# Kernel optimization log

Measured on AMD Instinct MI355X. Metric: run time of the kernel, lower is better.

The kernel has to match this reference:

```python
import jax, jax.numpy as jnp
import numpy as np
import math

N, L, S, H, E, D = 2, 2048, 2048, 16, 64, 64

def setup_inputs() -> dict:
    key = jax.random.key(0)
    kq, kk, kv = jax.random.split(key, 3)
    return {
        "queries": jax.random.normal(kq, (N, L, H, E), dtype=jnp.float32),
        "keys": jax.random.normal(kk, (N, S, H, E), dtype=jnp.float32),
        "values": jax.random.normal(kv, (N, S, H, D), dtype=jnp.float32),
        "attn_mask": jnp.zeros((L, S), dtype=jnp.float32),  # additive mask
    }

def reference(queries, keys, values, attn_mask):
    e = queries.shape[-1]
    softmax_temp = 1.0 / math.sqrt(e)  # self.softmax_temp is None -> 1/sqrt(E)
    # (N,L,H,E) x (N,S,H,E) -> (N,H,L,S)
    qk = jnp.einsum('nlhe,nshe->nhls', queries, keys)
    qk = qk + attn_mask  # additive mask broadcast over (N,H)
    att = jax.nn.softmax(softmax_temp * qk, axis=-1)
    # dropout rate 0.0 (eval) -> identity
    v = jnp.einsum('nhls,nshd->nlhd', att, values)
    return v
```

## Files before the change

### kernel.cpp

```cpp
#include <hip/hip_runtime.h>
#include <hip/hip_bf16.h>


typedef short bf16x8 __attribute__((ext_vector_type(8)));
typedef short short4v __attribute__((ext_vector_type(4)));
typedef unsigned uint2v __attribute__((ext_vector_type(2)));
typedef float f32x4 __attribute__((ext_vector_type(4)));

constexpr int Nb = 2, Lq = 2048, Sk = 2048, Hh = 16, Ee = 64, Dd = 64;
constexpr int BM = 128;
constexpr int BN = 64;
constexpr int NT = Sk / BN;
constexpr int KVB = Nb * Hh * NT * 16 * 64 / 256;
constexpr float SCALE_LOG2E = 0.125f * 1.4426950408889634f;

__device__ __forceinline__ short f2bf(float f) {
  union { float f; unsigned u; } v; v.f = f;
  unsigned r = (v.u + 0x7fffu + ((v.u >> 16) & 1u)) >> 16;
  return (short)r;
}

__device__ __forceinline__ unsigned pack_bf16x2(float a, float b) {
  union { __hip_bfloat162 h; unsigned u; } v;
  float2 f; f.x = a; f.y = b;
  v.h = __float22bfloat162_rn(f);
  return v.u;
}

__device__ __forceinline__ float bf_lo(unsigned u) { return __uint_as_float(u << 16); }
__device__ __forceinline__ float bf_hi(unsigned u) { return __uint_as_float(u & 0xffff0000u); }

__device__ __forceinline__ void async_copy16(const void* g, void* l) {
  __builtin_amdgcn_global_load_lds(
      (const __attribute__((address_space(1))) unsigned int*)g,
      (__attribute__((address_space(3))) unsigned int*)l, 16, 0, 0);
}

__global__ __launch_bounds__(256) void prep_all(const float* __restrict__ K,
                                                const float* __restrict__ V,
                                                const float* __restrict__ M,
                                                short* __restrict__ KVf,
                                                short* __restrict__ Mg) {
  if (blockIdx.x < KVB) {
    int gid = blockIdx.x * 256 + threadIdx.x;
    int l = gid & 63;
    int chunkid = gid >> 6;
    int ch = chunkid & 15;
    int t  = (chunkid >> 4) & 31;
    int nh = chunkid >> 9;
    int n = nh >> 4, h = nh & 15;
    int c = l & 15, quad = l >> 4;
    bf16x8 o;
    if (ch < 8) {
      int sb = ch >> 1, kc = ch & 1;
      int s = t * 64 + sb * 16 + c;
      int e0 = kc * 32 + quad * 8;
      const float* p = K + (((size_t)n * Sk + s) * Hh + h) * Ee + e0;
      float4 x = *(const float4*)(p);
      float4 y = *(const float4*)(p + 4);
      o[0] = f2bf(x.x); o[1] = f2bf(x.y); o[2] = f2bf(x.z); o[3] = f2bf(x.w);
      o[4] = f2bf(y.x); o[5] = f2bf(y.y); o[6] = f2bf(y.z); o[7] = f2bf(y.w);
    } else {
      int db = (ch - 8) >> 1, kc = (ch - 8) & 1;
      int d = db * 16 + c;
      int s0 = t * 64 + kc * 32 + quad * 8;
      const float* p = V + (((size_t)n * Sk + s0) * Hh + h) * Dd + d;
#pragma unroll
      for (int j = 0; j < 8; ++j) o[j] = f2bf(p[(size_t)j * Hh * Dd]);
    }
    *(bf16x8*)(KVf + (size_t)gid * 8) = o;
  } else {
    int u = (blockIdx.x - KVB) * 256 + threadIdx.x;
    int colg = u & 511;
    int row  = u >> 9;
    int qt = row >> 7, wv = (row >> 5) & 3, cb = (row >> 4) & 1, cc = row & 15;
    int t = colg >> 4, sb = (colg >> 2) & 3, quad = colg & 3;
    int lane = quad * 16 + cc;
    float4 mv = *(const float4*)(M + (size_t)row * Sk + colg * 4);
    short4v o;
    o[0] = f2bf(mv.x * SCALE_LOG2E); o[1] = f2bf(mv.y * SCALE_LOG2E);
    o[2] = f2bf(mv.z * SCALE_LOG2E); o[3] = f2bf(mv.w * SCALE_LOG2E);
    size_t gran = ((((size_t)((qt * 4 + wv) * 2 + cb) * 32 + t) * 4 + sb) * 64) + lane;
    *(short4v*)(Mg + gran * 4) = o;
  }
}

template <int NS>
__global__ __launch_bounds__(256, 4) void attn_fwd(
    const float* __restrict__ Q, const short* __restrict__ KVf,
    const short* __restrict__ Mg, float* __restrict__ P0,
    float* __restrict__ P1, float* __restrict__ rsW)
{
  __shared__ short KV[2][8192];
  __shared__ short Ps[4][1024];

  const int tid  = threadIdx.x;
  const int lane = tid & 63;
  const int w    = tid >> 6;
  const int quad = lane >> 4;
  const int c    = lane & 15;

  const int id   = blockIdx.x;
  const int slot = id >> 3;
  const int nh   = (id & 7) * 4 + (slot & 3);
  const int qt   = (slot >> 2) & 15;
  const int sp   = (NS == 2) ? (slot >> 6) : 0;
  const int n    = nh >> 4;
  const int h    = nh & 15;

  const int row0 = qt * BM + w * 32;
  const int t0 = sp * (NT / NS), tc = NT / NS;

  bf16x8 qfrag[2][2];
#pragma unroll
  for (int cb = 0; cb < 2; ++cb) {
    const float* qp = Q + (((size_t)n * Lq + (row0 + cb * 16 + c)) * Hh + h) * Ee;
#pragma unroll
    for (int kc = 0; kc < 2; ++kc) {
      const float* p = qp + kc * 32 + quad * 8;
      float4 x = *(const float4*)(p);
      float4 y = *(const float4*)(p + 4);
      bf16x8 f;
      f[0] = f2bf(x.x * SCALE_LOG2E); f[1] = f2bf(x.y * SCALE_LOG2E);
      f[2] = f2bf(x.z * SCALE_LOG2E); f[3] = f2bf(x.w * SCALE_LOG2E);
      f[4] = f2bf(y.x * SCALE_LOG2E); f[5] = f2bf(y.y * SCALE_LOG2E);
      f[6] = f2bf(y.z * SCALE_LOG2E); f[7] = f2bf(y.w * SCALE_LOG2E);
      qfrag[cb][kc] = f;
    }
  }

  f32x4 o[2][4];
#pragma unroll
  for (int cb = 0; cb < 2; ++cb)
#pragma unroll
    for (int db = 0; db < 4; ++db) { o[cb][db][0] = 0.f; o[cb][db][1] = 0.f; o[cb][db][2] = 0.f; o[cb][db][3] = 0.f; }
  float rs[2] = {0.f, 0.f};

  const short* kvt = KVf + (size_t)nh * NT * 8192;
  const short* mbase = Mg + (size_t)((qt * 4 + w) * 2) * 32768 + lane * 4;

#pragma unroll
  for (int i = 0; i < 4; ++i) {
    int ch = w * 4 + i;
    async_copy16(kvt + ((size_t)t0 * 8192) + ch * 512 + lane * 8, &KV[0][ch * 512 + lane * 8]);
  }
  __syncthreads();

  for (int tt = 0; tt < tc; ++tt) {
    const int t = t0 + tt;
    const int buf = tt & 1;

    uint2v mv[2][4];
#pragma unroll
    for (int cb = 0; cb < 2; ++cb)
#pragma unroll
      for (int sb = 0; sb < 4; ++sb)
        mv[cb][sb] = *(const uint2v*)(mbase + ((size_t)cb * 32 + t) * 1024 + sb * 256);

    if (tt + 1 < tc) {
      const short* gk = kvt + (size_t)(t + 1) * 8192;
#pragma unroll
      for (int i = 0; i < 4; ++i) {
        int ch = w * 4 + i;
        async_copy16(gk + ch * 512 + lane * 8, &KV[buf ^ 1][ch * 512 + lane * 8]);
      }
    }

    const short* kb = &KV[buf][0];

    f32x4 sacc[2][4];
#pragma unroll
    for (int cb = 0; cb < 2; ++cb)
#pragma unroll
      for (int sb = 0; sb < 4; ++sb) { sacc[cb][sb][0] = 0.f; sacc[cb][sb][1] = 0.f; sacc[cb][sb][2] = 0.f; sacc[cb][sb][3] = 0.f; }
#pragma unroll
    for (int kc = 0; kc < 2; ++kc) {
#pragma unroll
      for (int sb = 0; sb < 4; ++sb) {
        bf16x8 kfrag = *(const bf16x8*)&kb[(sb * 2 + kc) * 512 + lane * 8];
#pragma unroll
        for (int cb = 0; cb < 2; ++cb)
          sacc[cb][sb] = __builtin_amdgcn_mfma_f32_16x16x32_bf16(kfrag, qfrag[cb][kc], sacc[cb][sb], 0, 0, 0);
      }
    }

    bf16x8 pfrag[2][2];
#pragma unroll
    for (int cb = 0; cb < 2; ++cb) {
#pragma unroll
      for (int sb = 0; sb < 4; ++sb) {
        float p0 = __builtin_amdgcn_exp2f(sacc[cb][sb][0] + bf_lo(mv[cb][sb].x));
        float p1 = __builtin_amdgcn_exp2f(sacc[cb][sb][1] + bf_hi(mv[cb][sb].x));
        float p2 = __builtin_amdgcn_exp2f(sacc[cb][sb][2] + bf_lo(mv[cb][sb].y));
        float p3 = __builtin_amdgcn_exp2f(sacc[cb][sb][3] + bf_hi(mv[cb][sb].y));
        rs[cb] += (p0 + p1) + (p2 + p3);
        uint2v pv;
        pv.x = pack_bf16x2(p0, p1);
        pv.y = pack_bf16x2(p2, p3);
        int gp = ((4 * sb + quad) ^ c) * 4;
        *(uint2v*)&Ps[w][c * 64 + gp] = pv;
      }
#pragma unroll
      for (int kc = 0; kc < 2; ++kc) {
        int G0 = 8 * kc + 2 * quad;
        int ga = (G0 ^ c) * 4, gb = ((G0 + 1) ^ c) * 4;
        union { uint2v u[2]; bf16x8 f; } uu;
        uu.u[0] = *(const uint2v*)&Ps[w][c * 64 + ga];
        uu.u[1] = *(const uint2v*)&Ps[w][c * 64 + gb];
        pfrag[cb][kc] = uu.f;
      }
    }

#pragma unroll
    for (int kc = 0; kc < 2; ++kc) {
#pragma unroll
      for (int db = 0; db < 4; ++db) {
        bf16x8 vfrag = *(const bf16x8*)&kb[(8 + db * 2 + kc) * 512 + lane * 8];
#pragma unroll
        for (int cb = 0; cb < 2; ++cb)
          o[cb][db] = __builtin_amdgcn_mfma_f32_16x16x32_bf16(vfrag, pfrag[cb][kc], o[cb][db], 0, 0, 0);
      }
    }

    __syncthreads();
  }

  float* P = (sp == 0) ? P0 : P1;
#pragma unroll
  for (int cb = 0; cb < 2; ++cb) {
    float v = rs[cb];
    v += __shfl_xor(v, 16, 64);
    v += __shfl_xor(v, 32, 64);
    const int qrow = row0 + cb * 16 + c;
    if (quad == 0) rsW[(size_t)sp * 65536 + nh * 2048 + qrow] = v;
    float* op = P + (((size_t)n * Lq + qrow) * Hh + h) * Dd + quad * 4;
#pragma unroll
    for (int db = 0; db < 4; ++db) {
      float4 ov;
      ov.x = o[cb][db][0]; ov.y = o[cb][db][1];
      ov.z = o[cb][db][2]; ov.w = o[cb][db][3];
      *(float4*)(op + db * 16) = ov;
    }
  }
}

template <int NS>
__global__ __launch_bounds__(256) void combine(float* __restrict__ Out,
                                               const float* __restrict__ P1,
                                               const float* __restrict__ rsW) {
  int gid = blockIdx.x * 256 + threadIdx.x;
  size_t i4 = (size_t)gid * 4;
  int hh = (int)((i4 >> 6) & 15);
  int l  = (int)((i4 >> 10) & 2047);
  int nn = (int)(i4 >> 21);
  int nh = nn * 16 + hh;
  float rs = rsW[nh * 2048 + l];
  float4 v = *(const float4*)(Out + i4);
  if (NS == 2) {
    rs += rsW[65536 + (size_t)nh * 2048 + l];
    float4 b = *(const float4*)(P1 + i4);
    v.x += b.x; v.y += b.y; v.z += b.z; v.w += b.w;
  }
  float inv = 1.0f / rs;
  v.x *= inv; v.y *= inv; v.z *= inv; v.w *= inv;
  *(float4*)(Out + i4) = v;
}

extern "C" void kernel_launch(void* const* d_in, const int* in_sizes, int n_in,
                              void* d_out, int out_size, void* d_ws, size_t ws_size,
                              hipStream_t stream) {
  const float* Q   = (const float*)d_in[0];
  const float* K   = (const float*)d_in[1];
  const float* V   = (const float*)d_in[2];
  const float* Msk = (const float*)d_in[3];
  float* Out = (float*)d_out;

  short* KVf = (short*)d_ws;
  short* Mg  = KVf + (size_t)8388608;
  float* rsW = (float*)(Mg + (size_t)4194304);
  float* P1  = rsW + 131072;

  const size_t need2 = 16777216u + 8388608u + 524288u + 16777216u;
  const bool split = ws_size >= need2;

  prep_all<<<dim3(KVB + 4096), dim3(256), 0, stream>>>(K, V, Msk, KVf, Mg);

  if (split) {
    attn_fwd<2><<<dim3(1024), dim3(256), 0, stream>>>(Q, KVf, Mg, Out, P1, rsW);
    combine<2><<<dim3(4096), dim3(256), 0, stream>>>(Out, P1, rsW);
  } else {
    attn_fwd<1><<<dim3(512), dim3(256), 0, stream>>>(Q, KVf, Mg, Out, P1, rsW);
    combine<1><<<dim3(4096), dim3(256), 0, stream>>>(Out, P1, rsW);
  }
}
```

Before: 171.0 us.

## Drop LDS round-trip for P by using 16x16x16 MFMA and relayout V/mask

The PV product now uses the 16x16x16 bf16 MFMA, so the exponentiated score accumulator fragments feed directly as the B operand. This removes the per-wave LDS staging buffer for P and its write/read shuffle. The V and mask prep layouts are rearranged to match. The mask is now preloaded into the score accumulators as the initial value and prefetched one tile ahead into registers. The cost is twice as many smaller MFMA instructions for PV and more registers held by the mask prefetch.

Result: faster. 166.3 us (-2.8%).

```diff
diff --git a/kernel.cpp b/kernel.cpp
--- a/kernel.cpp
+++ b/kernel.cpp
@@ -5,13 +5,15 @@
 typedef short bf16x8 __attribute__((ext_vector_type(8)));
 typedef short short4v __attribute__((ext_vector_type(4)));
 typedef unsigned uint2v __attribute__((ext_vector_type(2)));
+typedef unsigned uint4v __attribute__((ext_vector_type(4)));
 typedef float f32x4 __attribute__((ext_vector_type(4)));
 
 constexpr int Nb = 2, Lq = 2048, Sk = 2048, Hh = 16, Ee = 64, Dd = 64;
 constexpr int BM = 128;
 constexpr int BN = 64;
 constexpr int NT = Sk / BN;
-constexpr int KVB = Nb * Hh * NT * 16 * 64 / 256;
+constexpr int KVB = 4096;
+constexpr int MSKB = 2048;
 constexpr float SCALE_LOG2E = 0.125f * 1.4426950408889634f;
 
 __device__ __forceinline__ short f2bf(float f) {
@@ -43,45 +45,59 @@
                                                 short* __restrict__ Mg) {
   if (blockIdx.x < KVB) {
     int gid = blockIdx.x * 256 + threadIdx.x;
-    int l = gid & 63;
-    int chunkid = gid >> 6;
-    int ch = chunkid & 15;
-    int t  = (chunkid >> 4) & 31;
-    int nh = chunkid >> 9;
+    int off8 = gid & 1023;
+    int t  = (gid >> 10) & 31;
+    int nh = gid >> 15;
     int n = nh >> 4, h = nh & 15;
-    int c = l & 15, quad = l >> 4;
-    bf16x8 o;
-    if (ch < 8) {
-      int sb = ch >> 1, kc = ch & 1;
-      int s = t * 64 + sb * 16 + c;
-      int e0 = kc * 32 + quad * 8;
-      const float* p = K + (((size_t)n * Sk + s) * Hh + h) * Ee + e0;
+    short* dst = KVf + ((size_t)(nh * NT + t)) * 8192 + off8 * 8;
+    if (off8 < 512) {
+      int ch = off8 >> 6;
+      int l  = off8 & 63;
+      int sb = ch >> 1, kc = ch & 1, c = l & 15, quad = l >> 4;
+      const float* p = K + (((size_t)n * Sk + (t * 64 + sb * 16 + c)) * Hh + h) * Ee
+                         + kc * 32 + quad * 8;
       float4 x = *(const float4*)(p);
       float4 y = *(const float4*)(p + 4);
+      bf16x8 o;
       o[0] = f2bf(x.x); o[1] = f2bf(x.y); o[2] = f2bf(x.z); o[3] = f2bf(x.w);
       o[4] = f2bf(y.x); o[5] = f2bf(y.y); o[6] = f2bf(y.z); o[7] = f2bf(y.w);
+      *(bf16x8*)dst = o;
     } else {
-      int db = (ch - 8) >> 1, kc = (ch - 8) & 1;
-      int d = db * 16 + c;
-      int s0 = t * 64 + kc * 32 + quad * 8;
-      const float* p = V + (((size_t)n * Sk + s0) * Hh + h) * Dd + d;
-#pragma unroll
-      for (int j = 0; j < 8; ++j) o[j] = f2bf(p[(size_t)j * Hh * Dd]);
-    }
-    *(bf16x8*)(KVf + (size_t)gid * 8) = o;
+      int pos = off8 - 512;
+      int vch = pos >> 5;
+      int l0  = (pos & 31) * 2;
+      int db = vch >> 2, sb = vch & 3;
+      bf16x8 o;
+#pragma unroll
+      for (int i = 0; i < 2; ++i) {
+        int l = l0 + i, c = l & 15, quad = l >> 4;
+        const float* p = V + (((size_t)n * Sk + (t * 64 + sb * 16 + quad * 4)) * Hh + h) * Dd
+                           + db * 16 + c;
+#pragma unroll
+        for (int j = 0; j < 4; ++j) o[i * 4 + j] = f2bf(p[(size_t)j * Hh * Dd]);
+      }
+      *(bf16x8*)dst = o;
+    }
   } else {
     int u = (blockIdx.x - KVB) * 256 + threadIdx.x;
-    int colg = u & 511;
-    int row  = u >> 9;
-    int qt = row >> 7, wv = (row >> 5) & 3, cb = (row >> 4) & 1, cc = row & 15;
-    int t = colg >> 4, sb = (colg >> 2) & 3, quad = colg & 3;
-    int lane = quad * 16 + cc;
-    float4 mv = *(const float4*)(M + (size_t)row * Sk + colg * 4);
-    short4v o;
-    o[0] = f2bf(mv.x * SCALE_LOG2E); o[1] = f2bf(mv.y * SCALE_LOG2E);
-    o[2] = f2bf(mv.z * SCALE_LOG2E); o[3] = f2bf(mv.w * SCALE_LOG2E);
-    size_t gran = ((((size_t)((qt * 4 + wv) * 2 + cb) * 32 + t) * 4 + sb) * 64) + lane;
-    *(short4v*)(Mg + gran * 4) = o;
+    int sub  = u & 3;
+    int lane = (u >> 2) & 63;
+    int t    = (u >> 8) & 31;
+    int qw   = u >> 13;
+    int cb = sub >> 1, sbp = sub & 1;
+    int c = lane & 15, quad = lane >> 4;
+    int row = (qw >> 2) * 128 + (qw & 3) * 32 + cb * 16 + c;
+    short o[8];
+#pragma unroll
+    for (int k = 0; k < 2; ++k) {
+      int sb = sbp * 2 + k;
+      float4 mv = *(const float4*)(M + (size_t)row * Sk + t * 64 + sb * 16 + quad * 4);
+      o[k * 4 + 0] = f2bf(mv.x * SCALE_LOG2E);
+      o[k * 4 + 1] = f2bf(mv.y * SCALE_LOG2E);
+      o[k * 4 + 2] = f2bf(mv.z * SCALE_LOG2E);
+      o[k * 4 + 3] = f2bf(mv.w * SCALE_LOG2E);
+    }
+    *(bf16x8*)(Mg + (size_t)u * 8) = *(const bf16x8*)o;
   }
 }
 
@@ -92,7 +108,6 @@
     float* __restrict__ P1, float* __restrict__ rsW)
 {
   __shared__ short KV[2][8192];
-  __shared__ short Ps[4][1024];
 
   const int tid  = threadIdx.x;
   const int lane = tid & 63;
@@ -137,42 +152,48 @@
   float rs[2] = {0.f, 0.f};
 
   const short* kvt = KVf + (size_t)nh * NT * 8192;
-  const short* mbase = Mg + (size_t)((qt * 4 + w) * 2) * 32768 + lane * 4;
+  const short* mbase = Mg + (size_t)(qt * 4 + w) * 65536 + lane * 32;
 
 #pragma unroll
   for (int i = 0; i < 4; ++i) {
-    int ch = w * 4 + i;
-    async_copy16(kvt + ((size_t)t0 * 8192) + ch * 512 + lane * 8, &KV[0][ch * 512 + lane * 8]);
-  }
+    int seg = w * 4 + i;
+    async_copy16(kvt + ((size_t)t0 * 8192) + seg * 512 + lane * 8, &KV[0][seg * 512 + lane * 8]);
+  }
+  uint4v mcur[4], mnxt[4];
+#pragma unroll
+  for (int i = 0; i < 4; ++i) mcur[i] = *(const uint4v*)(mbase + (size_t)t0 * 2048 + i * 8);
   __syncthreads();
 
   for (int tt = 0; tt < tc; ++tt) {
     const int t = t0 + tt;
     const int buf = tt & 1;
 
-    uint2v mv[2][4];
+    if (tt + 1 < tc) {
+      const short* gm = mbase + (size_t)(t + 1) * 2048;
+#pragma unroll
+      for (int i = 0; i < 4; ++i) mnxt[i] = *(const uint4v*)(gm + i * 8);
+      const short* gk = kvt + (size_t)(t + 1) * 8192;
+#pragma unroll
+      for (int i = 0; i < 4; ++i) {
+        int seg = w * 4 + i;
+        async_copy16(gk + seg * 512 + lane * 8, &KV[buf ^ 1][seg * 512 + lane * 8]);
+      }
+    }
+
+    const short* kb = &KV[buf][0];
+
+    f32x4 sacc[2][4];
 #pragma unroll
     for (int cb = 0; cb < 2; ++cb)
 #pragma unroll
-      for (int sb = 0; sb < 4; ++sb)
-        mv[cb][sb] = *(const uint2v*)(mbase + ((size_t)cb * 32 + t) * 1024 + sb * 256);
-
-    if (tt + 1 < tc) {
-      const short* gk = kvt + (size_t)(t + 1) * 8192;
-#pragma unroll
-      for (int i = 0; i < 4; ++i) {
-        int ch = w * 4 + i;
-        async_copy16(gk + ch * 512 + lane * 8, &KV[buf ^ 1][ch * 512 + lane * 8]);
-      }
-    }
-
-    const short* kb = &KV[buf][0];
-
-    f32x4 sacc[2][4];
-#pragma unroll
-    for (int cb = 0; cb < 2; ++cb)
-#pragma unroll
-      for (int sb = 0; sb < 4; ++sb) { sacc[cb][sb][0] = 0.f; sacc[cb][sb][1] = 0.f; sacc[cb][sb][2] = 0.f; sacc[cb][sb][3] = 0.f; }
+      for (int sbp = 0; sbp < 2; ++sbp) {
+        uint4v m = mcur[cb * 2 + sbp];
+        sacc[cb][sbp * 2 + 0][0] = bf_lo(m.x); sacc[cb][sbp * 2 + 0][1] = bf_hi(m.x);
+        sacc[cb][sbp * 2 + 0][2] = bf_lo(m.y); sacc[cb][sbp * 2 + 0][3] = bf_hi(m.y);
+        sacc[cb][sbp * 2 + 1][0] = bf_lo(m.z); sacc[cb][sbp * 2 + 1][1] = bf_hi(m.z);
+        sacc[cb][sbp * 2 + 1][2] = bf_lo(m.w); sacc[cb][sbp * 2 + 1][3] = bf_hi(m.w);
+      }
+
 #pragma unroll
     for (int kc = 0; kc < 2; ++kc) {
 #pragma unroll
@@ -184,45 +205,36 @@
       }
     }
 
-    bf16x8 pfrag[2][2];
-#pragma unroll
-    for (int cb = 0; cb < 2; ++cb) {
+    short4v pv[2][4];
+#pragma unroll
+    for (int cb = 0; cb < 2; ++cb)
 #pragma unroll
       for (int sb = 0; sb < 4; ++sb) {
-        float p0 = __builtin_amdgcn_exp2f(sacc[cb][sb][0] + bf_lo(mv[cb][sb].x));
-        float p1 = __builtin_amdgcn_exp2f(sacc[cb][sb][1] + bf_hi(mv[cb][sb].x));
-        float p2 = __builtin_amdgcn_exp2f(sacc[cb][sb][2] + bf_lo(mv[cb][sb].y));
-        float p3 = __builtin_amdgcn_exp2f(sacc[cb][sb][3] + bf_hi(mv[cb][sb].y));
+        float p0 = __builtin_amdgcn_exp2f(sacc[cb][sb][0]);
+        float p1 = __builtin_amdgcn_exp2f(sacc[cb][sb][1]);
+        float p2 = __builtin_amdgcn_exp2f(sacc[cb][sb][2]);
+        float p3 = __builtin_amdgcn_exp2f(sacc[cb][sb][3]);
         rs[cb] += (p0 + p1) + (p2 + p3);
-        uint2v pv;
-        pv.x = pack_bf16x2(p0, p1);
-        pv.y = pack_bf16x2(p2, p3);
-        int gp = ((4 * sb + quad) ^ c) * 4;
-        *(uint2v*)&Ps[w][c * 64 + gp] = pv;
-      }
-#pragma unroll
-      for (int kc = 0; kc < 2; ++kc) {
-        int G0 = 8 * kc + 2 * quad;
-        int ga = (G0 ^ c) * 4, gb = ((G0 + 1) ^ c) * 4;
-        union { uint2v u[2]; bf16x8 f; } uu;
-        uu.u[0] = *(const uint2v*)&Ps[w][c * 64 + ga];
-        uu.u[1] = *(const uint2v*)&Ps[w][c * 64 + gb];
-        pfrag[cb][kc] = uu.f;
-      }
-    }
-
-#pragma unroll
-    for (int kc = 0; kc < 2; ++kc) {
+        union { uint2v u; short4v s; } uu;
+        uu.u.x = pack_bf16x2(p0, p1);
+        uu.u.y = pack_bf16x2(p2, p3);
+        pv[cb][sb] = uu.s;
+      }
+
+#pragma unroll
+    for (int sb = 0; sb < 4; ++sb) {
 #pragma unroll
       for (int db = 0; db < 4; ++db) {
-        bf16x8 vfrag = *(const bf16x8*)&kb[(8 + db * 2 + kc) * 512 + lane * 8];
+        short4v vfrag = *(const short4v*)&kb[4096 + (db * 4 + sb) * 256 + lane * 4];
 #pragma unroll
         for (int cb = 0; cb < 2; ++cb)
-          o[cb][db] = __builtin_amdgcn_mfma_f32_16x16x32_bf16(vfrag, pfrag[cb][kc], o[cb][db], 0, 0, 0);
+          o[cb][db] = __builtin_amdgcn_mfma_f32_16x16x16bf16_1k(vfrag, pv[cb][sb], o[cb][db], 0, 0, 0);
       }
     }
 
     __syncthreads();
+#pragma unroll
+    for (int i = 0; i < 4; ++i) mcur[i] = mnxt[i];
   }
 
   float* P = (sp == 0) ? P0 : P1;
@@ -283,7 +295,7 @@
   const size_t need2 = 16777216u + 8388608u + 524288u + 16777216u;
   const bool split = ws_size >= need2;
 
-  prep_all<<<dim3(KVB + 4096), dim3(256), 0, stream>>>(K, V, Msk, KVf, Mg);
+  prep_all<<<dim3(KVB + MSKB), dim3(256), 0, stream>>>(K, V, Msk, KVf, Mg);
 
   if (split) {
     attn_fwd<2><<<dim3(1024), dim3(256), 0, stream>>>(Q, KVf, Mg, Out, P1, rsW);
```
